# Kernel tuning notes

Hardware: AMD Instinct MI355X
Metric: run time of the kernel (lower is better)

## Reference

```python
import jax, jax.numpy as jnp
import numpy as np

D_MODEL, D_K, D_V = 1024, 128, 128
B, S = 8, 2048


def setup_inputs() -> dict:
    key = jax.random.key(0)
    ks = jax.random.split(key, 10)
    scale = 1.0 / np.sqrt(D_MODEL)
    return {
        "inputs_q": jax.random.normal(ks[0], (B, S, D_MODEL), jnp.float32),
        "inputs_k": jax.random.normal(ks[1], (B, S, D_MODEL), jnp.float32),
        "inputs_v": jax.random.normal(ks[2], (B, S, D_MODEL), jnp.float32),
        "mask": jax.random.randint(ks[3], (B, 1, S), 0, 2, jnp.int32),
        "Wq": jax.random.normal(ks[4], (D_MODEL, D_K), jnp.float32) * scale,
        "bq": jnp.zeros((D_K,), jnp.float32),
        "Wk": jax.random.normal(ks[5], (D_MODEL, D_K), jnp.float32) * scale,
        "bk": jnp.zeros((D_K,), jnp.float32),
        "Wv": jax.random.normal(ks[6], (D_MODEL, D_V), jnp.float32) * scale,
        "bv": jnp.zeros((D_V,), jnp.float32),
    }


def reference(inputs_q, inputs_k, inputs_v, mask, Wq, bq, Wk, bk, Wv, bv):
    query = inputs_q @ Wq + bq            # [B,Sq,d_k]
    key = inputs_k @ Wk + bk              # [B,Sk,d_k]
    value = inputs_v @ Wv + bv            # [B,Sk,d_v]
    scores = jnp.einsum('bqd,bkd->bqk', query, key) / jnp.sqrt(jnp.float32(D_K))
    # original: mask==True means attend; inverted mask positions get -1e9
    mask_float = jnp.logical_not(mask.astype(bool)).astype(jnp.float32)  # [B,1,Sk]
    scores = scores + mask_float * (-1e9)
    attention_weights = jax.nn.softmax(scores, axis=-1)
    attention_weights = attention_weights * (1.0 - mask_float)
    output = jnp.einsum('bqk,bkv->bqv', attention_weights, value)
    return output
```

## Files before the change

kernel.cpp:

```cpp
#include <hip/hip_runtime.h>

#define L2E 1.44269504088896341f
#define SM_SHIFT 5.77078016355585f

typedef _Float16 h8 __attribute__((ext_vector_type(8)));
typedef float f4 __attribute__((ext_vector_type(4)));

__device__ __forceinline__ void gll16(const void* g, void* l) {
  __builtin_amdgcn_global_load_lds((const __attribute__((address_space(1))) void*)g,
                                   (__attribute__((address_space(3))) void*)l, 16, 0, 0);
}

__device__ __forceinline__ f4 mfma_h(h8 a, h8 b, f4 c) {
  return __builtin_amdgcn_mfma_f32_16x16x32_f16(a, b, c, 0, 0, 0);
}

__device__ __forceinline__ h8 pack8(const float4& a, const float4& b) {
  h8 hv;
  hv[0] = (_Float16)a.x; hv[1] = (_Float16)a.y; hv[2] = (_Float16)a.z; hv[3] = (_Float16)a.w;
  hv[4] = (_Float16)b.x; hv[5] = (_Float16)b.y; hv[6] = (_Float16)b.z; hv[7] = (_Float16)b.w;
  return hv;
}

__global__ void wt_prep(const float* __restrict__ Wq, const float* __restrict__ Wk,
                        const float* __restrict__ Wv, const int* __restrict__ maskp,
                        _Float16* __restrict__ Wt, _Float16* __restrict__ mh) {
  int z = blockIdx.y;
  const float* W = (z == 0) ? Wq : ((z == 1) ? Wk : Wv);
  _Float16* o = Wt + (size_t)z * 131072;
  int idx = blockIdx.x * 256 + threadIdx.x;
  int k = idx >> 7, n = idx & 127;
  o[(k >> 6) * 8192 + ((k >> 3) & 7) * 1024 + n * 8 + (k & 7)] = (_Float16)W[idx];
  if (z == 0 && idx < 16384) mh[idx] = (_Float16)(float)maskp[idx];
}

__global__ __launch_bounds__(256, 3) void proj_qkv(
    const float* __restrict__ Xq, const float* __restrict__ Xk, const float* __restrict__ Xv,
    const _Float16* __restrict__ Wt, const int* __restrict__ maskp,
    const float* __restrict__ bq, const float* __restrict__ bk, const float* __restrict__ bv,
    _Float16* __restrict__ Qh, _Float16* __restrict__ Kpk, _Float16* __restrict__ Vpk) {
  const int z = blockIdx.y;
  const float* X; const float* bias;
  if (z == 0) { X = Xq; bias = bq; }
  else if (z == 1) { X = Xk; bias = bk; }
  else { X = Xv; bias = bv; }
  const _Float16* Wz = Wt + (size_t)z * 131072;
  const int row0 = blockIdx.x * 64;
  const int tid = threadIdx.x;
  const int lane = tid & 63, wid = tid >> 6;
  const int wr = wid >> 1, wc = wid & 1;
  const int l15 = lane & 15, g = lane >> 4;

  __shared__ __align__(16) _Float16 Al[4096];
  __shared__ __align__(16) _Float16 Bl[2][8192];

  f4 acc[2][4];
#pragma unroll
  for (int i = 0; i < 2; i++)
#pragma unroll
    for (int j = 0; j < 4; j++) acc[i][j] = (f4){0.f, 0.f, 0.f, 0.f};

  float4 areg[2][2];
  const int ar_row = tid >> 3, ar_ko = tid & 7;
  auto loadA = [&](int t) {
#pragma unroll
    for (int it = 0; it < 2; it++) {
      const float* gp = X + (size_t)(row0 + it * 32 + ar_row) * 1024 + t * 64 + ar_ko * 8;
      areg[it][0] = *(const float4*)gp;
      areg[it][1] = *(const float4*)(gp + 4);
    }
  };
  auto writeA = [&]() {
#pragma unroll
    for (int it = 0; it < 2; it++) {
      int row = it * 32 + ar_row;
      *(h8*)&Al[(row * 8 + (ar_ko ^ (row & 7))) * 8] = pack8(areg[it][0], areg[it][1]);
    }
  };
  auto loadB = [&](int buf, int t) {
#pragma unroll
    for (int it = 0; it < 4; it++)
      gll16(Wz + t * 8192 + it * 2048 + tid * 8, &Bl[buf][it * 2048 + tid * 8]);
  };
  auto compute = [&](int buf) {
#pragma unroll
    for (int kc = 0; kc < 2; kc++) {
      int o = kc * 4 + g;
      h8 af[2], bf[4];
#pragma unroll
      for (int mf = 0; mf < 2; mf++) {
        int row = wr * 32 + mf * 16 + l15;
        af[mf] = *(const h8*)&Al[(row * 8 + (o ^ (row & 7))) * 8];
      }
#pragma unroll
      for (int nf = 0; nf < 4; nf++) {
        int col = wc * 64 + nf * 16 + l15;
        bf[nf] = *(const h8*)&Bl[buf][(o * 128 + col) * 8];
      }
#pragma unroll
      for (int mf = 0; mf < 2; mf++)
#pragma unroll
        for (int nf = 0; nf < 4; nf++)
          acc[mf][nf] = mfma_h(af[mf], bf[nf], acc[mf][nf]);
    }
  };

  loadA(0);
  loadB(0, 0);

  int cur = 0;
  for (int t = 0; t < 16; t++) {
    writeA();
    __syncthreads();
    if (t < 15) {
      loadA(t + 1);
      loadB(cur ^ 1, t + 1);
    }
    compute(cur);
    __syncthreads();
    cur ^= 1;
  }

  const float qscale = (z == 0) ? 0.08838834764831845f : 1.0f;
#pragma unroll
  for (int nf = 0; nf < 4; nf++) {
    int colb = wc * 64 + nf * 16 + l15;
    float bv_ = bias[colb];
#pragma unroll
    for (int mf = 0; mf < 2; mf++)
#pragma unroll
      for (int jj = 0; jj < 4; jj++) {
        int m = row0 + wr * 32 + mf * 16 + g * 4 + jj;
        float v = (acc[mf][nf][jj] + bv_) * qscale;
        if (z == 2) v *= (float)maskp[m];
        _Float16 hv = (_Float16)v;
        if (z == 0) Qh[m * 128 + colb] = hv;
        else if (z == 1) Kpk[(m >> 6) * 8192 + (colb >> 3) * 512 + (m & 63) * 8 + (colb & 7)] = hv;
        else Vpk[(m >> 6) * 8192 + ((m & 63) >> 3) * 1024 + colb * 8 + (m & 7)] = hv;
      }
  }
}

__global__ __launch_bounds__(256, 2) void attn_fwd(
    const _Float16* __restrict__ Qh, const _Float16* __restrict__ Kpk,
    const _Float16* __restrict__ Vpk, const _Float16* __restrict__ maskh,
    float* __restrict__ Out) {
  const int bi = blockIdx.x & 7;
  const int qt = blockIdx.x >> 3;
  const int tid = threadIdx.x;
  const int lane = tid & 63, wid = tid >> 6;
  const int l15 = lane & 15, g = lane >> 4;
  const int qg = wid & 1;
  const int kh = wid >> 1;

  __shared__ __align__(16) _Float16 Kt[16384];
  __shared__ __align__(16) _Float16 Pl[4][1024];

  const size_t mb = (size_t)bi * 2048;
  const int q0 = qt * 32 + qg * 16;

  h8 qf[4];
#pragma unroll
  for (int c = 0; c < 4; c++)
    qf[c] = *(const h8*)(Qh + (mb + q0 + l15) * 128 + c * 32 + g * 8);

  const _Float16* Kb = Kpk + (size_t)bi * 262144;
  const _Float16* Vb = Vpk + (size_t)bi * 262144;
  const _Float16* mhp = maskh + mb;

  f4 oacc[8];
#pragma unroll
  for (int i = 0; i < 8; i++) oacc[i] = (f4){0.f, 0.f, 0.f, 0.f};
  f4 lacc = (f4){0.f, 0.f, 0.f, 0.f};

  h8 kreg[8], mregC[2], mregN[2], vf[2][8];
#pragma unroll
  for (int it = 0; it < 8; it++)
    kreg[it] = *(const h8*)(Kb + (it * 256 + tid) * 8);
#pragma unroll
  for (int kc2 = 0; kc2 < 2; kc2++)
    mregC[kc2] = *(const h8*)(mhp + kh * 64 + kc2 * 32 + g * 8);

  for (int s = 0; s < 16; s++) {
#pragma unroll
    for (int it = 0; it < 8; it++) {
      int wg = it * 256 + tid;
      *(h8*)&Kt[(wg ^ ((wg >> 6) & 7)) * 8] = kreg[it];
    }
    __syncthreads();

    if (s < 15) {
      const _Float16* gk = Kb + (size_t)(s + 1) * 16384;
#pragma unroll
      for (int it = 0; it < 8; it++)
        kreg[it] = *(const h8*)(gk + (it * 256 + tid) * 8);
#pragma unroll
      for (int kc2 = 0; kc2 < 2; kc2++)
        mregN[kc2] = *(const h8*)(mhp + (s + 1) * 128 + kh * 64 + kc2 * 32 + g * 8);
    }

    {
      const _Float16* vch = Vb + (size_t)(2 * s + kh) * 8192;
#pragma unroll
      for (int kc2 = 0; kc2 < 2; kc2++)
#pragma unroll
        for (int nf = 0; nf < 8; nf++)
          vf[kc2][nf] = *(const h8*)(vch + (((kc2 * 4 + g) * 128) + nf * 16 + l15) * 8);
    }

    f4 sc[4];
#pragma unroll
    for (int nf = 0; nf < 4; nf++) sc[nf] = (f4){0.f, 0.f, 0.f, 0.f};
    __builtin_amdgcn_s_setprio(1);
#pragma unroll
    for (int c = 0; c < 4; c++) {
      int dblk = c * 4 + g;
#pragma unroll
      for (int nf = 0; nf < 4; nf++) {
        int key64 = nf * 16 + l15;
        int kg = kh * 1024 + dblk * 64 + (key64 ^ (dblk & 7));
        h8 bfr = *(const h8*)&Kt[kg * 8];
        sc[nf] = mfma_h(qf[c], bfr, sc[nf]);
      }
    }
    __builtin_amdgcn_s_setprio(0);

#pragma unroll
    for (int nf = 0; nf < 4; nf++) {
      int key64 = nf * 16 + l15;
      int kb = key64 >> 3, j = key64 & 7;
#pragma unroll
      for (int jj = 0; jj < 4; jj++) {
        int q = g * 4 + jj;
        float p = __builtin_amdgcn_exp2f(sc[nf][jj] * L2E - SM_SHIFT);
        Pl[wid][((kb * 16 + (q ^ (kb & 7))) << 3) + j] = (_Float16)p;
      }
    }

    __builtin_amdgcn_s_setprio(1);
#pragma unroll
    for (int kc2 = 0; kc2 < 2; kc2++) {
      int kbp = kc2 * 4 + g;
      h8 pa = *(const h8*)&Pl[wid][((kbp * 16 + (l15 ^ (kbp & 7))) << 3)];
      lacc = mfma_h(pa, mregC[kc2], lacc);
#pragma unroll
      for (int nf = 0; nf < 8; nf++)
        oacc[nf] = mfma_h(pa, vf[kc2][nf], oacc[nf]);
    }
    __builtin_amdgcn_s_setprio(0);
    if (s < 15) {
      mregC[0] = mregN[0];
      mregC[1] = mregN[1];
    }
    __syncthreads();
  }

  float* red = (float*)Kt;
  if (kh == 1) {
    int base = qg * 2304;
#pragma unroll
    for (int nf = 0; nf < 8; nf++)
#pragma unroll
      for (int jj = 0; jj < 4; jj++)
        red[base + (nf * 4 + jj) * 64 + lane] = oacc[nf][jj];
#pragma unroll
    for (int jj = 0; jj < 4; jj++)
      red[base + 2048 + jj * 64 + lane] = lacc[jj];
  }
  __syncthreads();
  if (kh == 0) {
    int base = qg * 2304;
#pragma unroll
    for (int nf = 0; nf < 8; nf++)
#pragma unroll
      for (int jj = 0; jj < 4; jj++)
        oacc[nf][jj] += red[base + (nf * 4 + jj) * 64 + lane];
#pragma unroll
    for (int jj = 0; jj < 4; jj++)
      lacc[jj] += red[base + 2048 + jj * 64 + lane];

    float inv[4];
#pragma unroll
    for (int jj = 0; jj < 4; jj++)
      inv[jj] = (lacc[jj] > 0.f) ? 1.0f / lacc[jj] : 0.0f;
#pragma unroll
    for (int nf = 0; nf < 8; nf++)
#pragma unroll
      for (int jj = 0; jj < 4; jj++)
        Out[(mb + q0 + g * 4 + jj) * 128 + nf * 16 + l15] = oacc[nf][jj] * inv[jj];
  }
}

extern "C" void kernel_launch(void* const* d_in, const int* in_sizes, int n_in,
                              void* d_out, int out_size, void* d_ws, size_t ws_size,
                              hipStream_t stream) {
  const float* Xq = (const float*)d_in[0];
  const float* Xk = (const float*)d_in[1];
  const float* Xv = (const float*)d_in[2];
  const int* mask = (const int*)d_in[3];
  const float* Wq = (const float*)d_in[4];
  const float* bq = (const float*)d_in[5];
  const float* Wk = (const float*)d_in[6];
  const float* bk = (const float*)d_in[7];
  const float* Wv = (const float*)d_in[8];
  const float* bv = (const float*)d_in[9];
  float* Out = (float*)d_out;

  char* ws = (char*)d_ws;
  _Float16* Qh    = (_Float16*)(ws);
  _Float16* Kpk   = (_Float16*)(ws + 4194304);
  _Float16* Vpk   = (_Float16*)(ws + 8388608);
  _Float16* Wt    = (_Float16*)(ws + 12582912);
  _Float16* maskh = (_Float16*)(ws + 13369344);

  wt_prep<<<dim3(512, 3), 256, 0, stream>>>(Wq, Wk, Wv, mask, Wt, maskh);
  proj_qkv<<<dim3(256, 3), 256, 0, stream>>>(Xq, Xk, Xv, Wt, mask, bq, bk, bv, Qh, Kpk, Vpk);
  attn_fwd<<<dim3(512), 256, 0, stream>>>(Qh, Kpk, Vpk, maskh, Out);
}
```

Before: 86.75 us.

## Double-buffer K tiles in LDS and vectorize weight/mask prep

The attention kernel now keeps two K tiles in shared memory. It writes the next tile into the alternate buffer while computing on the current one, which removes one barrier per iteration, and it prefetches global K two steps ahead. The weight-transpose prep kernel handles four elements per thread with packed half4 stores and vectorized mask conversion, so it launches a quarter of the blocks. The cost is doubled LDS use for K (64KB), which may reduce occupancy below the two blocks per CU the launch bounds target.

New measurement: 108.6 us. +25.2%, slower.

```diff
diff --git a/kernel.cpp b/kernel.cpp
--- a/kernel.cpp
+++ b/kernel.cpp
@@ -4,6 +4,7 @@
 #define SM_SHIFT 5.77078016355585f
 
 typedef _Float16 h8 __attribute__((ext_vector_type(8)));
+typedef _Float16 h4 __attribute__((ext_vector_type(4)));
 typedef float f4 __attribute__((ext_vector_type(4)));
 
 __device__ __forceinline__ void gll16(const void* g, void* l) {
@@ -28,10 +29,19 @@
   int z = blockIdx.y;
   const float* W = (z == 0) ? Wq : ((z == 1) ? Wk : Wv);
   _Float16* o = Wt + (size_t)z * 131072;
-  int idx = blockIdx.x * 256 + threadIdx.x;
-  int k = idx >> 7, n = idx & 127;
-  o[(k >> 6) * 8192 + ((k >> 3) & 7) * 1024 + n * 8 + (k & 7)] = (_Float16)W[idx];
-  if (z == 0 && idx < 16384) mh[idx] = (_Float16)(float)maskp[idx];
+  int w = blockIdx.x * 256 + threadIdx.x;
+  int n = w & 127, kg = w >> 7;
+  h4 hv;
+#pragma unroll
+  for (int i = 0; i < 4; i++) hv[i] = (_Float16)W[(kg * 4 + i) * 128 + n];
+  *(h4*)&o[(kg >> 4) * 8192 + ((kg >> 1) & 7) * 1024 + n * 8 + (kg & 1) * 4] = hv;
+  if (z == 0 && w < 4096) {
+    int4 mi = *(const int4*)&maskp[w * 4];
+    h4 mv;
+    mv[0] = (_Float16)(float)mi.x; mv[1] = (_Float16)(float)mi.y;
+    mv[2] = (_Float16)(float)mi.z; mv[3] = (_Float16)(float)mi.w;
+    *(h4*)&mh[w * 4] = mv;
+  }
 }
 
 __global__ __launch_bounds__(256, 3) void proj_qkv(
@@ -153,7 +163,7 @@
   const int qg = wid & 1;
   const int kh = wid >> 1;
 
-  __shared__ __align__(16) _Float16 Kt[16384];
+  __shared__ __align__(16) _Float16 Kt[2][16384];
   __shared__ __align__(16) _Float16 Pl[4][1024];
 
   const size_t mb = (size_t)bi * 2048;
@@ -174,26 +184,37 @@
   f4 lacc = (f4){0.f, 0.f, 0.f, 0.f};
 
   h8 kreg[8], mregC[2], mregN[2], vf[2][8];
+
 #pragma unroll
   for (int it = 0; it < 8; it++)
     kreg[it] = *(const h8*)(Kb + (it * 256 + tid) * 8);
 #pragma unroll
+  for (int it = 0; it < 8; it++) {
+    int wg = it * 256 + tid;
+    *(h8*)&Kt[0][(wg ^ ((wg >> 6) & 7)) * 8] = kreg[it];
+  }
+#pragma unroll
+  for (int it = 0; it < 8; it++)
+    kreg[it] = *(const h8*)(Kb + 16384 + (it * 256 + tid) * 8);
+#pragma unroll
   for (int kc2 = 0; kc2 < 2; kc2++)
     mregC[kc2] = *(const h8*)(mhp + kh * 64 + kc2 * 32 + g * 8);
-
+  __syncthreads();
+
+  int cur = 0;
   for (int s = 0; s < 16; s++) {
-#pragma unroll
-    for (int it = 0; it < 8; it++) {
-      int wg = it * 256 + tid;
-      *(h8*)&Kt[(wg ^ ((wg >> 6) & 7)) * 8] = kreg[it];
-    }
-    __syncthreads();
-
     if (s < 15) {
-      const _Float16* gk = Kb + (size_t)(s + 1) * 16384;
-#pragma unroll
-      for (int it = 0; it < 8; it++)
-        kreg[it] = *(const h8*)(gk + (it * 256 + tid) * 8);
+#pragma unroll
+      for (int it = 0; it < 8; it++) {
+        int wg = it * 256 + tid;
+        *(h8*)&Kt[cur ^ 1][(wg ^ ((wg >> 6) & 7)) * 8] = kreg[it];
+      }
+      if (s < 14) {
+        const _Float16* gk = Kb + (size_t)(s + 2) * 16384;
+#pragma unroll
+        for (int it = 0; it < 8; it++)
+          kreg[it] = *(const h8*)(gk + (it * 256 + tid) * 8);
+      }
 #pragma unroll
       for (int kc2 = 0; kc2 < 2; kc2++)
         mregN[kc2] = *(const h8*)(mhp + (s + 1) * 128 + kh * 64 + kc2 * 32 + g * 8);
@@ -219,7 +240,7 @@
       for (int nf = 0; nf < 4; nf++) {
         int key64 = nf * 16 + l15;
         int kg = kh * 1024 + dblk * 64 + (key64 ^ (dblk & 7));
-        h8 bfr = *(const h8*)&Kt[kg * 8];
+        h8 bfr = *(const h8*)&Kt[cur][kg * 8];
         sc[nf] = mfma_h(qf[c], bfr, sc[nf]);
       }
     }
@@ -253,9 +274,10 @@
       mregC[1] = mregN[1];
     }
     __syncthreads();
-  }
-
-  float* red = (float*)Kt;
+    cur ^= 1;
+  }
+
+  float* red = (float*)&Kt[0][0];
   if (kh == 1) {
     int base = qg * 2304;
 #pragma unroll
@@ -313,7 +335,7 @@
   _Float16* Wt    = (_Float16*)(ws + 12582912);
   _Float16* maskh = (_Float16*)(ws + 13369344);
 
-  wt_prep<<<dim3(512, 3), 256, 0, stream>>>(Wq, Wk, Wv, mask, Wt, maskh);
+  wt_prep<<<dim3(128, 3), 256, 0, stream>>>(Wq, Wk, Wv, mask, Wt, maskh);
   proj_qkv<<<dim3(256, 3), 256, 0, stream>>>(Xq, Xk, Xv, Wt, mask, bq, bk, bv, Qh, Kpk, Vpk);
   attn_fwd<<<dim3(512), 256, 0, stream>>>(Qh, Kpk, Vpk, maskh, Out);
 }
```
